# Optimization experiments

Hardware: AMD Instinct MI355X
Metric: run time of the kernel (lower is better)

## Reference

```python
import jax, jax.numpy as jnp
import numpy as np

N_NODES = 100000


def gcn_conv(x, W, b, src, dst, n):
    h = x @ W  # transform first (PyG GCNConv order), smaller edge traffic
    loops = jnp.arange(n, dtype=src.dtype)
    s = jnp.concatenate([src, loops])
    d = jnp.concatenate([dst, loops])
    deg = jax.ops.segment_sum(jnp.ones_like(d, dtype=h.dtype), d, num_segments=n)
    dinv = jnp.where(deg > 0, jax.lax.rsqrt(deg), 0.0)
    norm = dinv[s] * dinv[d]  # [E+N]
    msg = h[s] * norm[:, None]  # gather + scale
    out = jax.ops.segment_sum(msg, d, num_segments=n)  # scatter-add
    return out + b


def setup_inputs() -> dict:
    key = jax.random.key(0)
    ks = jax.random.split(key, 8)
    x = jax.random.normal(ks[0], (N_NODES, 256), dtype=jnp.float32)
    edge_index = jax.random.randint(ks[1], (2, 1600000), 0, N_NODES, dtype=jnp.int64)
    pos_edge_index = jax.random.randint(ks[2], (2, 200000), 0, N_NODES, dtype=jnp.int64)
    neg_edge_index = jax.random.randint(ks[3], (2, 200000), 0, N_NODES, dtype=jnp.int64)
    W1 = jax.random.normal(ks[4], (256, 128), dtype=jnp.float32) * (1.0 / np.sqrt(256))
    b1 = jnp.zeros((128,), dtype=jnp.float32)
    W2 = jax.random.normal(ks[5], (128, 8), dtype=jnp.float32) * (1.0 / np.sqrt(128))
    b2 = jnp.zeros((8,), dtype=jnp.float32)
    return {"x": x, "edge_index": edge_index, "pos_edge_index": pos_edge_index,
            "neg_edge_index": neg_edge_index, "W1": W1, "b1": b1, "W2": W2, "b2": b2}


def reference(x, edge_index, pos_edge_index, neg_edge_index, W1, b1, W2, b2):
    n = x.shape[0]
    src, dst = edge_index[0], edge_index[1]
    h = jax.nn.relu(gcn_conv(x, W1, b1, src, dst, n))
    z = gcn_conv(h, W2, b2, src, dst, n)  # [N, 8]
    ei = jnp.concatenate([pos_edge_index, neg_edge_index], axis=-1)
    return jnp.sum(z[ei[0]] * z[ei[1]], axis=-1)  # [E_pos + E_neg]
```

## Files before the change

kernel.cpp:

```cpp
#include <hip/hip_runtime.h>

constexpr int N   = 100000;
constexpr int E   = 1600000;
constexpr int EP  = 200000;
constexpr int ES  = 400000;
constexpr int CAP = 64;
constexpr int XG2 = 128;
constexpr int DR2 = (N + XG2 - 1) / XG2;
constexpr int SEGCAP = 14336;
constexpr int EPB = 8192;
constexpr int PBS = 1024;
constexpr int NPB = (E + EPB - 1) / EPB;
constexpr int BSTR = 264;

typedef _Float16 f16x8 __attribute__((ext_vector_type(8)));
typedef _Float16 f16x4 __attribute__((ext_vector_type(4)));
typedef _Float16 f16x2 __attribute__((ext_vector_type(2)));
typedef float    f32x4 __attribute__((ext_vector_type(4)));

__global__ __launch_bounds__(1024) void partition_edges(const int* __restrict__ ei,
                                                        int* __restrict__ gcnt,
                                                        unsigned* __restrict__ eb) {
    __shared__ int lh[XG2];
    __shared__ int rk[XG2];
    const int tid = threadIdx.x;
    const int e0  = blockIdx.x * EPB;
    if (tid < XG2) lh[tid] = 0;
    __syncthreads();
#pragma unroll
    for (int i = 0; i < EPB; i += PBS) {
        const int e = e0 + i + tid;
        if (e < E) {
            const int d = ei[E + e];
            atomicAdd(&lh[d / DR2], 1);
        }
    }
    __syncthreads();
    if (tid < XG2) rk[tid] = atomicAdd(&gcnt[tid], lh[tid]);
    __syncthreads();
#pragma unroll
    for (int i = 0; i < EPB; i += PBS) {
        const int e = e0 + i + tid;
        if (e < E) {
            const int s   = ei[e];
            const int d   = ei[E + e];
            const int g   = d / DR2;
            const int rel = d - g * DR2;
            const int p   = atomicAdd(&rk[g], 1);
            if (p < SEGCAP)
                eb[(size_t)g * SEGCAP + p] = ((unsigned)rel << 17) | (unsigned)s;
        }
    }
}

__global__ __launch_bounds__(1024) void fill_csr(const unsigned* __restrict__ eb,
                                                 const int* __restrict__ gcnt,
                                                 int* __restrict__ cnt,
                                                 int* __restrict__ rp,
                                                 int* __restrict__ colc) {
    __shared__ int hcnt[1024];
    __shared__ int wsum[16];
    __shared__ unsigned stage[SEGCAP];
    const int g   = blockIdx.x;
    const int tid = threadIdx.x;
    const int cg  = min(gcnt[g], SEGCAP);
    const unsigned* seg = eb + (size_t)g * SEGCAP;

    hcnt[tid] = 0;
    __syncthreads();
    for (int i = tid; i < cg; i += 1024)
        atomicAdd(&hcnt[seg[i] >> 17], 1);
    __syncthreads();

    const int c    = hcnt[tid];
    const int lane = tid & 63;
    const int wid  = tid >> 6;
    int incl = c;
#pragma unroll
    for (int off = 1; off < 64; off <<= 1) {
        const int v = __shfl_up(incl, off);
        if (lane >= off) incl += v;
    }
    if (lane == 63) wsum[wid] = incl;
    __syncthreads();
    if (tid < 16) {
        int v = wsum[tid];
#pragma unroll
        for (int off = 1; off < 16; off <<= 1) {
            const int u = __shfl_up(v, off);
            if (tid >= off) v += u;
        }
        wsum[tid] = v;
    }
    __syncthreads();
    const int excl = incl - c + (wid ? wsum[wid - 1] : 0);

    const int base = g * DR2;
    if (tid < DR2 && base + tid < N) {
        cnt[base + tid] = c;
        rp [base + tid] = g * SEGCAP + excl;
    }
    __syncthreads();
    hcnt[tid] = excl;
    __syncthreads();

    for (int i = tid; i < cg; i += 1024) {
        const unsigned pk = seg[i];
        const int p = atomicAdd(&hcnt[pk >> 17], 1);
        stage[p] = pk & 0x1FFFFu;
    }
    __syncthreads();
    for (int i = tid; i < cg; i += 1024)
        colc[(size_t)g * SEGCAP + i] = (int)stage[i];
}

__global__ __launch_bounds__(256) void w1_transpose(const float* __restrict__ W1,
                                                    _Float16* __restrict__ W1T) {
    const int n = blockIdx.x;
    const int k = threadIdx.x;
    W1T[n * 256 + k] = (_Float16)W1[(size_t)k * 128 + n];
}

__global__ __launch_bounds__(256) void gemm1_mfma(const float* __restrict__ X,
                                                  const _Float16* __restrict__ W1T,
                                                  _Float16* __restrict__ H) {
    __shared__ _Float16 Bs[128][BSTR];

    const int tid  = threadIdx.x;
    const int wave = tid >> 6;
    const int lane = tid & 63;
    const int m16  = lane & 15;
    const int quad = lane >> 4;
    const int rowBase = blockIdx.x * 256 + wave * 64;

#pragma unroll
    for (int i = 0; i < 16; ++i) {
        const int c  = tid + 256 * i;
        const int n  = c >> 5;
        const int kb = (c & 31) * 16;
        *(f16x8*)((char*)&Bs[n][0] + kb) = *(const f16x8*)((const char*)W1T + (size_t)c * 16);
    }
    __syncthreads();

    f32x4 acc[4][8] = {};
    f32x4 avA[8];

    auto loadA = [&](int k0) {
#pragma unroll
        for (int m = 0; m < 4; ++m) {
            int gr = rowBase + m * 16 + m16;
            gr = gr < N ? gr : N - 1;
            const f32x4* p = (const f32x4*)&X[(size_t)gr * 256 + k0 + quad * 8];
            avA[2 * m]     = __builtin_nontemporal_load(p);
            avA[2 * m + 1] = __builtin_nontemporal_load(p + 1);
        }
    };

    loadA(0);
    for (int k0 = 0; k0 < 256; k0 += 32) {
        f16x8 af[4];
#pragma unroll
        for (int m = 0; m < 4; ++m) {
            f16x8 h;
            h[0] = (_Float16)avA[2*m][0];   h[1] = (_Float16)avA[2*m][1];
            h[2] = (_Float16)avA[2*m][2];   h[3] = (_Float16)avA[2*m][3];
            h[4] = (_Float16)avA[2*m+1][0]; h[5] = (_Float16)avA[2*m+1][1];
            h[6] = (_Float16)avA[2*m+1][2]; h[7] = (_Float16)avA[2*m+1][3];
            af[m] = h;
        }
        if (k0 + 32 < 256) loadA(k0 + 32);
#pragma unroll
        for (int nt = 0; nt < 8; ++nt) {
            const f16x8 bf = *(const f16x8*)&Bs[nt * 16 + m16][k0 + quad * 8];
#pragma unroll
            for (int m = 0; m < 4; ++m)
                acc[m][nt] = __builtin_amdgcn_mfma_f32_16x16x32_f16(af[m], bf, acc[m][nt], 0, 0, 0);
        }
    }

#pragma unroll
    for (int m = 0; m < 4; ++m)
#pragma unroll
        for (int nt = 0; nt < 8; ++nt)
#pragma unroll
            for (int r = 0; r < 4; ++r) {
                const int gm = rowBase + m * 16 + quad * 4 + r;
                if (gm < N) H[(size_t)gm * 128 + nt * 16 + m16] = (_Float16)acc[m][nt][r];
            }
}

__global__ __launch_bounds__(256) void agg1_gemm2(const _Float16* __restrict__ H,
                                                  const int* __restrict__ cnt,
                                                  const int* __restrict__ rp,
                                                  const int* __restrict__ colc,
                                                  const float* __restrict__ b1,
                                                  const float* __restrict__ W2,
                                                  float* __restrict__ Z) {
    const int n    = (blockIdx.x * blockDim.x + threadIdx.x) >> 6;
    const int lane = threadIdx.x & 63;
    if (n >= N) return;
    const int c = min(cnt[n], CAP);
    const int rpn = rp[n];

    int sv = n;
    if (lane < c) sv = colc[rpn + lane];
    const float dvw = rsqrtf((float)cnt[sv] + 1.0f);
    const float dv  = (lane <= c) ? dvw : 0.0f;

    const _Float16* hbase = H + lane * 2;
    const int ned4 = (c + 1 + 3) & ~3;

    f16x2 va[4]; float wa[4];
#pragma unroll
    for (int t = 0; t < 4; ++t) {
        const int   e = min(t, 63);
        const int   s = __shfl(sv, e);
        wa[t]         = __shfl(dv, e);
        va[t] = *(const f16x2*)&hbase[(size_t)s * 128];
    }
    float ax = 0.f, ay = 0.f;
    for (int j = 4; j < ned4; j += 4) {
        f16x2 vb[4]; float wb[4];
#pragma unroll
        for (int t = 0; t < 4; ++t) {
            const int   e = min(j + t, 63);
            const int   s = __shfl(sv, e);
            wb[t]         = __shfl(dv, e);
            vb[t] = *(const f16x2*)&hbase[(size_t)s * 128];
        }
#pragma unroll
        for (int t = 0; t < 4; ++t) {
            ax = fmaf(wa[t], (float)va[t][0], ax);
            ay = fmaf(wa[t], (float)va[t][1], ay);
            va[t] = vb[t]; wa[t] = wb[t];
        }
    }
#pragma unroll
    for (int t = 0; t < 4; ++t) {
        ax = fmaf(wa[t], (float)va[t][0], ax);
        ay = fmaf(wa[t], (float)va[t][1], ay);
    }

    const float dn = __shfl(dv, c);
    const float2 b = *(const float2*)&b1[lane * 2];
    const float hr0 = fmaxf(ax * dn + b.x, 0.f);
    const float hr1 = fmaxf(ay * dn + b.y, 0.f);

    const float4 wa0 = *(const float4*)&W2[(size_t)(lane * 2) * 8];
    const float4 wa1 = *(const float4*)&W2[(size_t)(lane * 2) * 8 + 4];
    const float4 wb0 = *(const float4*)&W2[(size_t)(lane * 2 + 1) * 8];
    const float4 wb1 = *(const float4*)&W2[(size_t)(lane * 2 + 1) * 8 + 4];
    float p[8];
    p[0] = hr0 * wa0.x + hr1 * wb0.x;
    p[1] = hr0 * wa0.y + hr1 * wb0.y;
    p[2] = hr0 * wa0.z + hr1 * wb0.z;
    p[3] = hr0 * wa0.w + hr1 * wb0.w;
    p[4] = hr0 * wa1.x + hr1 * wb1.x;
    p[5] = hr0 * wa1.y + hr1 * wb1.y;
    p[6] = hr0 * wa1.z + hr1 * wb1.z;
    p[7] = hr0 * wa1.w + hr1 * wb1.w;
#pragma unroll
    for (int off = 32; off > 0; off >>= 1)
#pragma unroll
        for (int j = 0; j < 8; ++j) p[j] += __shfl_xor(p[j], off);
    if (lane == 0) {
        *(float4*)&Z[(size_t)n * 8]     = make_float4(p[0], p[1], p[2], p[3]);
        *(float4*)&Z[(size_t)n * 8 + 4] = make_float4(p[4], p[5], p[6], p[7]);
    }
}

__global__ __launch_bounds__(256) void agg2(const float* __restrict__ Z,
                                            const int* __restrict__ cnt,
                                            const int* __restrict__ rp,
                                            const int* __restrict__ colc,
                                            const float* __restrict__ b2,
                                            float* __restrict__ ZA) {
    const int t = blockIdx.x * blockDim.x + threadIdx.x;
    const int n = t >> 3;
    const int f = t & 7;
    if (n >= N) return;
    const int c   = min(cnt[n], CAP);
    const int rpn = rp[n];

    float acc = 0.f;
    float zv[4], wv[4];
#pragma unroll
    for (int tt = 0; tt < 4; ++tt) {
        const int s = (tt < c) ? colc[rpn + tt] : n;
        wv[tt] = (tt < c) ? rsqrtf((float)cnt[s] + 1.0f) : 0.0f;
        zv[tt] = Z[(size_t)s * 8 + f];
    }
    for (int j = 4; j + 4 <= c + 4; j += 4) {
        float zb[4], wb[4];
#pragma unroll
        for (int tt = 0; tt < 4; ++tt) {
            const int jt = j + tt;
            const int s  = (jt < c) ? colc[rpn + jt] : n;
            wb[tt] = (jt < c) ? rsqrtf((float)cnt[s] + 1.0f) : 0.0f;
            zb[tt] = Z[(size_t)s * 8 + f];
        }
#pragma unroll
        for (int tt = 0; tt < 4; ++tt) {
            acc = fmaf(wv[tt], zv[tt], acc);
            zv[tt] = zb[tt]; wv[tt] = wb[tt];
        }
    }
#pragma unroll
    for (int tt = 0; tt < 4; ++tt) acc = fmaf(wv[tt], zv[tt], acc);

    const float dn = rsqrtf((float)c + 1.0f);
    const float zn = Z[(size_t)n * 8 + f];
    ZA[(size_t)n * 8 + f] = (acc + dn * zn) * dn + b2[f];
}

__global__ __launch_bounds__(256) void score(const float* __restrict__ ZA,
                                             const int* __restrict__ pe,
                                             const int* __restrict__ ne,
                                             float* __restrict__ out) {
    const int e = blockIdx.x * blockDim.x + threadIdx.x;
    if (e >= ES) return;
    int a, b;
    if (e < EP) { a = pe[e];      b = pe[EP + e]; }
    else        { a = ne[e - EP]; b = ne[e];      }
    const float4 xa0 = *(const float4*)&ZA[(size_t)a * 8];
    const float4 xa1 = *(const float4*)&ZA[(size_t)a * 8 + 4];
    const float4 xb0 = *(const float4*)&ZA[(size_t)b * 8];
    const float4 xb1 = *(const float4*)&ZA[(size_t)b * 8 + 4];
    out[e] = xa0.x * xb0.x + xa0.y * xb0.y + xa0.z * xb0.z + xa0.w * xb0.w +
             xa1.x * xb1.x + xa1.y * xb1.y + xa1.z * xb1.z + xa1.w * xb1.w;
}


extern "C" void kernel_launch(void* const* d_in, const int* in_sizes, int n_in,
                              void* d_out, int out_size, void* d_ws, size_t ws_size,
                              hipStream_t stream) {
    const float* x  = (const float*)d_in[0];
    const int*   ei = (const int*)d_in[1];
    const int*   pe = (const int*)d_in[2];
    const int*   ne = (const int*)d_in[3];
    const float* W1 = (const float*)d_in[4];
    const float* b1 = (const float*)d_in[5];
    const float* W2 = (const float*)d_in[6];
    const float* b2 = (const float*)d_in[7];
    float* out = (float*)d_out;

    char* ws = (char*)d_ws;
    size_t off = 0;
    auto carve = [&](size_t bytes) {
        char* p = ws + off;
        off += (bytes + 255) & ~(size_t)255;
        return p;
    };
    int*       gcnt = (int*)      carve((size_t)XG2 * sizeof(int));
    int*       cnt  = (int*)      carve((size_t)N * sizeof(int));
    int*       rp   = (int*)      carve((size_t)N * sizeof(int));
    unsigned*  eb   = (unsigned*) carve((size_t)XG2 * SEGCAP * sizeof(unsigned));
    int*       colc = (int*)      carve((size_t)XG2 * SEGCAP * sizeof(int));
    _Float16*  H    = (_Float16*) carve((size_t)N * 128 * sizeof(_Float16));
    float*     Z    = (float*)    carve((size_t)N * 8 * sizeof(float));
    float*     ZA   = (float*)    carve((size_t)N * 8 * sizeof(float));
    _Float16*  W1T  = (_Float16*) carve((size_t)128 * 256 * sizeof(_Float16));

    hipMemsetAsync(gcnt, 0, (size_t)XG2 * sizeof(int), stream);
    partition_edges<<<NPB, PBS, 0, stream>>>(ei, gcnt, eb);
    w1_transpose   <<<128, 256, 0, stream>>>(W1, W1T);
    fill_csr       <<<XG2, 1024, 0, stream>>>(eb, gcnt, cnt, rp, colc);
    gemm1_mfma     <<<(N + 255) / 256, 256, 0, stream>>>(x, W1T, H);
    agg1_gemm2     <<<((size_t)N * 64 + 255) / 256, 256, 0, stream>>>(H, cnt, rp, colc, b1, W2, Z);
    agg2           <<<((size_t)N * 8 + 255) / 256, 256, 0, stream>>>(Z, cnt, rp, colc, b2, ZA);
    score          <<<(ES + 255) / 256, 256, 0, stream>>>(ZA, pe, ne, out);
}
```

Baseline: 357.4 us.

## Precompute degree-normalization array and restructure layer-1 aggregation with wave-uniform indices

Computes rsqrt(deg+1) once per node in fill_csr and stores it in a dinv array, which both aggregation kernels now read in place of recomputing rsqrt from cnt. agg1_gemm2 makes the node index, count and row pointer wave-uniform with readfirstlane, and replaces the per-lane colc load plus shuffle broadcast with uniform loads of colc and dinv. Its gather pipeline also widens from 4 to 8 edges in flight. The aim is to cut shuffle traffic and ALU work and to raise memory-level parallelism on the H gather, at the cost of one extra array write and more registers.

```diff
diff --git a/kernel.cpp b/kernel.cpp
--- a/kernel.cpp
+++ b/kernel.cpp
@@ -57,6 +57,7 @@
                                                  const int* __restrict__ gcnt,
                                                  int* __restrict__ cnt,
                                                  int* __restrict__ rp,
+                                                 float* __restrict__ dinv,
                                                  int* __restrict__ colc) {
     __shared__ int hcnt[1024];
     __shared__ int wsum[16];
@@ -97,8 +98,9 @@
 
     const int base = g * DR2;
     if (tid < DR2 && base + tid < N) {
-        cnt[base + tid] = c;
-        rp [base + tid] = g * SEGCAP + excl;
+        cnt [base + tid] = c;
+        rp  [base + tid] = g * SEGCAP + excl;
+        dinv[base + tid] = rsqrtf((float)c + 1.0f);
     }
     __syncthreads();
     hcnt[tid] = excl;
@@ -193,63 +195,62 @@
                                                   const int* __restrict__ cnt,
                                                   const int* __restrict__ rp,
                                                   const int* __restrict__ colc,
+                                                  const float* __restrict__ dinv,
                                                   const float* __restrict__ b1,
                                                   const float* __restrict__ W2,
                                                   float* __restrict__ Z) {
-    const int n    = (blockIdx.x * blockDim.x + threadIdx.x) >> 6;
+    const int nw   = (blockIdx.x * blockDim.x + threadIdx.x) >> 6;
     const int lane = threadIdx.x & 63;
-    if (n >= N) return;
-    const int c = min(cnt[n], CAP);
-    const int rpn = rp[n];
-
-    int sv = n;
-    if (lane < c) sv = colc[rpn + lane];
-    const float dvw = rsqrtf((float)cnt[sv] + 1.0f);
-    const float dv  = (lane <= c) ? dvw : 0.0f;
+    if (nw >= N) return;
+    const int n   = __builtin_amdgcn_readfirstlane(nw);
+    const int c   = min(__builtin_amdgcn_readfirstlane(cnt[n]), CAP);
+    const int rpn = __builtin_amdgcn_readfirstlane(rp[n]);
+    const float dn = dinv[n];
 
     const _Float16* hbase = H + lane * 2;
-    const int ned4 = (c + 1 + 3) & ~3;
-
-    f16x2 va[4]; float wa[4];
-#pragma unroll
-    for (int t = 0; t < 4; ++t) {
-        const int   e = min(t, 63);
-        const int   s = __shfl(sv, e);
-        wa[t]         = __shfl(dv, e);
-        va[t] = *(const f16x2*)&hbase[(size_t)s * 128];
-    }
-    float ax = 0.f, ay = 0.f;
-    for (int j = 4; j < ned4; j += 4) {
-        f16x2 vb[4]; float wb[4];
-#pragma unroll
-        for (int t = 0; t < 4; ++t) {
-            const int   e = min(j + t, 63);
-            const int   s = __shfl(sv, e);
-            wb[t]         = __shfl(dv, e);
-            vb[t] = *(const f16x2*)&hbase[(size_t)s * 128];
-        }
-#pragma unroll
-        for (int t = 0; t < 4; ++t) {
-            ax = fmaf(wa[t], (float)va[t][0], ax);
-            ay = fmaf(wa[t], (float)va[t][1], ay);
-            va[t] = vb[t]; wa[t] = wb[t];
-        }
-    }
-#pragma unroll
-    for (int t = 0; t < 4; ++t) {
-        ax = fmaf(wa[t], (float)va[t][0], ax);
-        ay = fmaf(wa[t], (float)va[t][1], ay);
-    }
-
-    const float dn = __shfl(dv, c);
-    const float2 b = *(const float2*)&b1[lane * 2];
-    const float hr0 = fmaxf(ax * dn + b.x, 0.f);
-    const float hr1 = fmaxf(ay * dn + b.y, 0.f);
-
+
+    const float2 b   = *(const float2*)&b1[lane * 2];
     const float4 wa0 = *(const float4*)&W2[(size_t)(lane * 2) * 8];
     const float4 wa1 = *(const float4*)&W2[(size_t)(lane * 2) * 8 + 4];
     const float4 wb0 = *(const float4*)&W2[(size_t)(lane * 2 + 1) * 8];
     const float4 wb1 = *(const float4*)&W2[(size_t)(lane * 2 + 1) * 8 + 4];
+
+    f16x2 va[8]; float wa[8];
+#pragma unroll
+    for (int t = 0; t < 8; ++t) {
+        const int ec = t < c ? t : c;
+        const int s  = (ec < c) ? colc[rpn + ec] : n;
+        wa[t] = (t <= c) ? dinv[s] : 0.f;
+        va[t] = *(const f16x2*)&hbase[(size_t)s * 128];
+    }
+    float ax = 0.f, ay = 0.f;
+    const int tot8 = (c + 1 + 7) & ~7;
+    for (int j = 8; j < tot8; j += 8) {
+        f16x2 vb[8]; float wb[8];
+#pragma unroll
+        for (int t = 0; t < 8; ++t) {
+            const int e  = j + t;
+            const int ec = e < c ? e : c;
+            const int s  = (ec < c) ? colc[rpn + ec] : n;
+            wb[t] = (e <= c) ? dinv[s] : 0.f;
+            vb[t] = *(const f16x2*)&hbase[(size_t)s * 128];
+        }
+#pragma unroll
+        for (int t = 0; t < 8; ++t) {
+            ax = fmaf(wa[t], (float)va[t][0], ax);
+            ay = fmaf(wa[t], (float)va[t][1], ay);
+            va[t] = vb[t]; wa[t] = wb[t];
+        }
+    }
+#pragma unroll
+    for (int t = 0; t < 8; ++t) {
+        ax = fmaf(wa[t], (float)va[t][0], ax);
+        ay = fmaf(wa[t], (float)va[t][1], ay);
+    }
+
+    const float hr0 = fmaxf(ax * dn + b.x, 0.f);
+    const float hr1 = fmaxf(ay * dn + b.y, 0.f);
+
     float p[8];
     p[0] = hr0 * wa0.x + hr1 * wb0.x;
     p[1] = hr0 * wa0.y + hr1 * wb0.y;
@@ -273,6 +274,7 @@
                                             const int* __restrict__ cnt,
                                             const int* __restrict__ rp,
                                             const int* __restrict__ colc,
+                                            const float* __restrict__ dinv,
                                             const float* __restrict__ b2,
                                             float* __restrict__ ZA) {
     const int t = blockIdx.x * blockDim.x + threadIdx.x;
@@ -287,7 +289,7 @@
 #pragma unroll
     for (int tt = 0; tt < 4; ++tt) {
         const int s = (tt < c) ? colc[rpn + tt] : n;
-        wv[tt] = (tt < c) ? rsqrtf((float)cnt[s] + 1.0f) : 0.0f;
+        wv[tt] = (tt < c) ? dinv[s] : 0.0f;
         zv[tt] = Z[(size_t)s * 8 + f];
     }
     for (int j = 4; j + 4 <= c + 4; j += 4) {
@@ -296,7 +298,7 @@
         for (int tt = 0; tt < 4; ++tt) {
             const int jt = j + tt;
             const int s  = (jt < c) ? colc[rpn + jt] : n;
-            wb[tt] = (jt < c) ? rsqrtf((float)cnt[s] + 1.0f) : 0.0f;
+            wb[tt] = (jt < c) ? dinv[s] : 0.0f;
             zb[tt] = Z[(size_t)s * 8 + f];
         }
 #pragma unroll
@@ -308,7 +310,7 @@
 #pragma unroll
     for (int tt = 0; tt < 4; ++tt) acc = fmaf(wv[tt], zv[tt], acc);
 
-    const float dn = rsqrtf((float)c + 1.0f);
+    const float dn = dinv[n];
     const float zn = Z[(size_t)n * 8 + f];
     ZA[(size_t)n * 8 + f] = (acc + dn * zn) * dn + b2[f];
 }
@@ -354,6 +356,7 @@
     int*       gcnt = (int*)      carve((size_t)XG2 * sizeof(int));
     int*       cnt  = (int*)      carve((size_t)N * sizeof(int));
     int*       rp   = (int*)      carve((size_t)N * sizeof(int));
+    float*     dinv = (float*)    carve((size_t)N * sizeof(float));
     unsigned*  eb   = (unsigned*) carve((size_t)XG2 * SEGCAP * sizeof(unsigned));
     int*       colc = (int*)      carve((size_t)XG2 * SEGCAP * sizeof(int));
     _Float16*  H    = (_Float16*) carve((size_t)N * 128 * sizeof(_Float16));
@@ -364,9 +367,9 @@
     hipMemsetAsync(gcnt, 0, (size_t)XG2 * sizeof(int), stream);
     partition_edges<<<NPB, PBS, 0, stream>>>(ei, gcnt, eb);
     w1_transpose   <<<128, 256, 0, stream>>>(W1, W1T);
-    fill_csr       <<<XG2, 1024, 0, stream>>>(eb, gcnt, cnt, rp, colc);
+    fill_csr       <<<XG2, 1024, 0, stream>>>(eb, gcnt, cnt, rp, dinv, colc);
     gemm1_mfma     <<<(N + 255) / 256, 256, 0, stream>>>(x, W1T, H);
-    agg1_gemm2     <<<((size_t)N * 64 + 255) / 256, 256, 0, stream>>>(H, cnt, rp, colc, b1, W2, Z);
-    agg2           <<<((size_t)N * 8 + 255) / 256, 256, 0, stream>>>(Z, cnt, rp, colc, b2, ZA);
+    agg1_gemm2     <<<((size_t)N * 64 + 255) / 256, 256, 0, stream>>>(H, cnt, rp, colc, dinv, b1, W2, Z);
+    agg2           <<<((size_t)N * 8 + 255) / 256, 256, 0, stream>>>(Z, cnt, rp, colc, dinv, b2, ZA);
     score          <<<(ES + 255) / 256, 256, 0, stream>>>(ZA, pe, ne, out);
 }
```

New measurement: 348.7 us. -2.4%, faster.
